# Kernel optimization log

Hardware: AMD Instinct MI355X
Metric: run time of the kernel (lower is better)

## Reference

```python
import jax, jax.numpy as jnp
import numpy as np

NUM_NODES = 100000
HIDDEN = 128
NUM_EDGES = 625000


def setup_inputs() -> dict:
    key = jax.random.key(0)
    k_emb, k_edge = jax.random.split(key)
    node_ids = jnp.arange(NUM_NODES, dtype=jnp.int64 if jax.config.jax_enable_x64 else jnp.int32)
    edge_index = jax.random.randint(k_edge, (2, NUM_EDGES), 0, NUM_NODES, dtype=jnp.int32)
    emb_weight = jax.random.normal(k_emb, (NUM_NODES, HIDDEN), dtype=jnp.float32)
    return {"node_ids": node_ids, "edge_index": edge_index, "emb_weight": emb_weight}


def reference(node_ids, edge_index, emb_weight):
    # sources = node_ids[edge_index[0]]; vs = emb[sources]  -> [E, H] gather
    sources = node_ids[edge_index[0]]
    vs = emb_weight[sources]  # [E, H]
    tgt = edge_index[1]
    # scatter_mean over dim 0: segment-sum then divide by per-target counts
    sums = jax.ops.segment_sum(vs, tgt, num_segments=NUM_NODES)  # [N, H]
    counts = jax.ops.segment_sum(jnp.ones((vs.shape[0],), dtype=vs.dtype), tgt,
                                 num_segments=NUM_NODES)  # [N]
    # empty segments -> 0 (matches torch_scatter scatter_mean)
    return sums / jnp.maximum(counts, 1.0)[:, None]
```

## Files before the change

kernel.cpp:

```cpp
#include <hip/hip_runtime.h>


#define NUM_NODES 100000
#define HIDDEN    128
#define NUM_EDGES 625000
#define CAP       32

typedef float vfloat4 __attribute__((ext_vector_type(4)));

__global__ __launch_bounds__(256) void bucket_kernel(
    const int* __restrict__ node_ids,
    const int* __restrict__ src,
    const int* __restrict__ tgt,
    int* __restrict__ cnt,
    int* __restrict__ buckets)
{
    int e = blockIdx.x * blockDim.x + threadIdx.x;
    if (e >= NUM_EDGES) return;
    int t   = tgt[e];
    int pos = atomicAdd(&cnt[t], 1);
    if (pos < CAP)
        buckets[t * CAP + pos] = node_ids[src[e]];
}

__global__ __launch_bounds__(256) void gather_kernel(
    const int* __restrict__ cnt, const int* __restrict__ buckets,
    const float* __restrict__ emb, float* __restrict__ out)
{
    int gid  = blockIdx.x * blockDim.x + threadIdx.x;
    int n    = gid >> 5;
    int lane = gid & 31;
    if (n >= NUM_NODES) return;

    int c   = cnt[n];
    int m   = (c < CAP) ? c : CAP;
    const int* b = buckets + n * CAP;

    float4 acc0 = make_float4(0.f, 0.f, 0.f, 0.f);
    float4 acc1 = make_float4(0.f, 0.f, 0.f, 0.f);
    int i = 0;
    for (; i + 3 < m; i += 4) {
        int s0 = b[i + 0];
        int s1 = b[i + 1];
        int s2 = b[i + 2];
        int s3 = b[i + 3];
        const float4 a  = *reinterpret_cast<const float4*>(emb + (size_t)s0 * HIDDEN + lane * 4);
        const float4 bb = *reinterpret_cast<const float4*>(emb + (size_t)s1 * HIDDEN + lane * 4);
        const float4 cc = *reinterpret_cast<const float4*>(emb + (size_t)s2 * HIDDEN + lane * 4);
        const float4 dd = *reinterpret_cast<const float4*>(emb + (size_t)s3 * HIDDEN + lane * 4);
        acc0.x += a.x + bb.x; acc0.y += a.y + bb.y; acc0.z += a.z + bb.z; acc0.w += a.w + bb.w;
        acc1.x += cc.x + dd.x; acc1.y += cc.y + dd.y; acc1.z += cc.z + dd.z; acc1.w += cc.w + dd.w;
    }
    for (; i < m; ++i) {
        int s0 = b[i];
        const float4 a = *reinterpret_cast<const float4*>(emb + (size_t)s0 * HIDDEN + lane * 4);
        acc0.x += a.x; acc0.y += a.y; acc0.z += a.z; acc0.w += a.w;
    }
    float inv = (c > 0) ? 1.0f / (float)c : 0.0f;
    vfloat4 r;
    r.x = (acc0.x + acc1.x) * inv;
    r.y = (acc0.y + acc1.y) * inv;
    r.z = (acc0.z + acc1.z) * inv;
    r.w = (acc0.w + acc1.w) * inv;
    __builtin_nontemporal_store(r,
        reinterpret_cast<vfloat4*>(out + (size_t)n * HIDDEN + lane * 4));
}

extern "C" void kernel_launch(void* const* d_in, const int* in_sizes, int n_in,
                              void* d_out, int out_size, void* d_ws, size_t ws_size,
                              hipStream_t stream) {
    const int*   node_ids = (const int*)d_in[0];
    const int*   edge_idx = (const int*)d_in[1];
    const float* emb      = (const float*)d_in[2];
    float*       out      = (float*)d_out;

    const int* edge_src = edge_idx;
    const int* edge_tgt = edge_idx + NUM_EDGES;

    char* ws = (char*)d_ws;
    int* cnt     = (int*)(ws + 0);
    int* buckets = (int*)(ws + 400000);

    (void)hipMemsetAsync(cnt, 0, NUM_NODES * sizeof(int), stream);

    {
        int grid = (NUM_EDGES + 255) / 256;
        bucket_kernel<<<grid, 256, 0, stream>>>(node_ids, edge_src, edge_tgt,
                                                cnt, buckets);
    }
    {
        long long total = (long long)NUM_NODES * 32;
        int grid = (int)((total + 255) / 256);
        gather_kernel<<<grid, 256, 0, stream>>>(cnt, buckets, emb, out);
    }
}
```

Measured before the change: 172.0 us.

## Convert embeddings to bf16 in prep pass and gather half-width rows

Adds a cast pass, fused into the bucketing kernel, that rounds the embedding table to bf16 in workspace. The gather then reads 256-byte rows with 16 lanes per node, each accumulating 8 values in fp32. The intent is to halve the random-gather traffic. The cost is an extra full read of the fp32 table plus a bf16 write every call, and reduced input precision that may exceed the tolerance.

```diff
diff --git a/kernel.cpp b/kernel.cpp
--- a/kernel.cpp
+++ b/kernel.cpp
@@ -5,65 +5,95 @@
 #define HIDDEN    128
 #define NUM_EDGES 625000
 #define CAP       32
+#define CAST_ITEMS (NUM_NODES * HIDDEN / 8)
+#define PREP_ITEMS (CAST_ITEMS + NUM_EDGES)
 
 typedef float vfloat4 __attribute__((ext_vector_type(4)));
 
-__global__ __launch_bounds__(256) void bucket_kernel(
+__device__ __forceinline__ unsigned bf16_rne(float f) {
+    unsigned x = __float_as_uint(f);
+    return (x + 0x7FFFu + ((x >> 16) & 1u)) >> 16;
+}
+
+__global__ __launch_bounds__(256) void prep_kernel(
     const int* __restrict__ node_ids,
     const int* __restrict__ src,
     const int* __restrict__ tgt,
+    const float* __restrict__ emb,
     int* __restrict__ cnt,
-    int* __restrict__ buckets)
+    int* __restrict__ buckets,
+    uint4* __restrict__ emb16)
 {
-    int e = blockIdx.x * blockDim.x + threadIdx.x;
-    if (e >= NUM_EDGES) return;
-    int t   = tgt[e];
-    int pos = atomicAdd(&cnt[t], 1);
-    if (pos < CAP)
-        buckets[t * CAP + pos] = node_ids[src[e]];
+    int i = blockIdx.x * blockDim.x + threadIdx.x;
+    if (i < CAST_ITEMS) {
+        const float4* ev = reinterpret_cast<const float4*>(emb);
+        float4 a = ev[i * 2 + 0];
+        float4 b = ev[i * 2 + 1];
+        uint4 o;
+        o.x = bf16_rne(a.x) | (bf16_rne(a.y) << 16);
+        o.y = bf16_rne(a.z) | (bf16_rne(a.w) << 16);
+        o.z = bf16_rne(b.x) | (bf16_rne(b.y) << 16);
+        o.w = bf16_rne(b.z) | (bf16_rne(b.w) << 16);
+        emb16[i] = o;
+    } else if (i < PREP_ITEMS) {
+        int e   = i - CAST_ITEMS;
+        int t   = tgt[e];
+        int pos = atomicAdd(&cnt[t], 1);
+        if (pos < CAP)
+            buckets[t * CAP + pos] = node_ids[src[e]];
+    }
 }
 
 __global__ __launch_bounds__(256) void gather_kernel(
     const int* __restrict__ cnt, const int* __restrict__ buckets,
-    const float* __restrict__ emb, float* __restrict__ out)
+    const uint4* __restrict__ emb16, float* __restrict__ out)
 {
     int gid  = blockIdx.x * blockDim.x + threadIdx.x;
-    int n    = gid >> 5;
-    int lane = gid & 31;
+    int n    = gid >> 4;
+    int lane = gid & 15;
     if (n >= NUM_NODES) return;
 
-    int c   = cnt[n];
-    int m   = (c < CAP) ? c : CAP;
+    int c = cnt[n];
+    int m = (c < CAP) ? c : CAP;
     const int* b = buckets + n * CAP;
 
-    float4 acc0 = make_float4(0.f, 0.f, 0.f, 0.f);
-    float4 acc1 = make_float4(0.f, 0.f, 0.f, 0.f);
+    float acc[8] = {0,0,0,0,0,0,0,0};
+
+    auto accum = [&](uint4 u) {
+        acc[0] += __uint_as_float(u.x << 16);
+        acc[1] += __uint_as_float(u.x & 0xFFFF0000u);
+        acc[2] += __uint_as_float(u.y << 16);
+        acc[3] += __uint_as_float(u.y & 0xFFFF0000u);
+        acc[4] += __uint_as_float(u.z << 16);
+        acc[5] += __uint_as_float(u.z & 0xFFFF0000u);
+        acc[6] += __uint_as_float(u.w << 16);
+        acc[7] += __uint_as_float(u.w & 0xFFFF0000u);
+    };
+
     int i = 0;
     for (; i + 3 < m; i += 4) {
         int s0 = b[i + 0];
         int s1 = b[i + 1];
         int s2 = b[i + 2];
         int s3 = b[i + 3];
-        const float4 a  = *reinterpret_cast<const float4*>(emb + (size_t)s0 * HIDDEN + lane * 4);
-        const float4 bb = *reinterpret_cast<const float4*>(emb + (size_t)s1 * HIDDEN + lane * 4);
-        const float4 cc = *reinterpret_cast<const float4*>(emb + (size_t)s2 * HIDDEN + lane * 4);
-        const float4 dd = *reinterpret_cast<const float4*>(emb + (size_t)s3 * HIDDEN + lane * 4);
-        acc0.x += a.x + bb.x; acc0.y += a.y + bb.y; acc0.z += a.z + bb.z; acc0.w += a.w + bb.w;
-        acc1.x += cc.x + dd.x; acc1.y += cc.y + dd.y; acc1.z += cc.z + dd.z; acc1.w += cc.w + dd.w;
+        uint4 u0 = emb16[(size_t)s0 * 16 + lane];
+        uint4 u1 = emb16[(size_t)s1 * 16 + lane];
+        uint4 u2 = emb16[(size_t)s2 * 16 + lane];
+        uint4 u3 = emb16[(size_t)s3 * 16 + lane];
+        accum(u0); accum(u1); accum(u2); accum(u3);
     }
     for (; i < m; ++i) {
-        int s0 = b[i];
-        const float4 a = *reinterpret_cast<const float4*>(emb + (size_t)s0 * HIDDEN + lane * 4);
-        acc0.x += a.x; acc0.y += a.y; acc0.z += a.z; acc0.w += a.w;
+        uint4 u = emb16[(size_t)b[i] * 16 + lane];
+        accum(u);
     }
+
     float inv = (c > 0) ? 1.0f / (float)c : 0.0f;
-    vfloat4 r;
-    r.x = (acc0.x + acc1.x) * inv;
-    r.y = (acc0.y + acc1.y) * inv;
-    r.z = (acc0.z + acc1.z) * inv;
-    r.w = (acc0.w + acc1.w) * inv;
-    __builtin_nontemporal_store(r,
-        reinterpret_cast<vfloat4*>(out + (size_t)n * HIDDEN + lane * 4));
+    vfloat4 r0, r1;
+    r0.x = acc[0] * inv; r0.y = acc[1] * inv; r0.z = acc[2] * inv; r0.w = acc[3] * inv;
+    r1.x = acc[4] * inv; r1.y = acc[5] * inv; r1.z = acc[6] * inv; r1.w = acc[7] * inv;
+    float* o = out + (size_t)n * HIDDEN + lane * 8;
+    __builtin_nontemporal_store(r0, reinterpret_cast<vfloat4*>(o));
+    __builtin_nontemporal_store(r1, reinterpret_cast<vfloat4*>(o + 4));
 }
 
 extern "C" void kernel_launch(void* const* d_in, const int* in_sizes, int n_in,
@@ -78,19 +108,20 @@
     const int* edge_tgt = edge_idx + NUM_EDGES;
 
     char* ws = (char*)d_ws;
-    int* cnt     = (int*)(ws + 0);
-    int* buckets = (int*)(ws + 400000);
+    int*   cnt     = (int*)(ws + 0);
+    int*   buckets = (int*)(ws + 400000);
+    uint4* emb16   = (uint4*)(ws + 13200000);
 
     (void)hipMemsetAsync(cnt, 0, NUM_NODES * sizeof(int), stream);
 
     {
-        int grid = (NUM_EDGES + 255) / 256;
-        bucket_kernel<<<grid, 256, 0, stream>>>(node_ids, edge_src, edge_tgt,
-                                                cnt, buckets);
+        int grid = (PREP_ITEMS + 255) / 256;
+        prep_kernel<<<grid, 256, 0, stream>>>(node_ids, edge_src, edge_tgt,
+                                              emb, cnt, buckets, emb16);
     }
     {
-        long long total = (long long)NUM_NODES * 32;
+        long long total = (long long)NUM_NODES * 16;
         int grid = (int)((total + 255) / 256);
-        gather_kernel<<<grid, 256, 0, stream>>>(cnt, buckets, emb, out);
+        gather_kernel<<<grid, 256, 0, stream>>>(cnt, buckets, emb16, out);
     }
 }
```

New measurement: 167.0 us. 1.03x faster.
